# Performance work log

Hardware: AMD Instinct MI355X
Metric: run time of the kernel (lower is better)

## Reference

```python
import jax, jax.numpy as jnp
import numpy as np

B, S = 1, 2048
HIDDEN = 4096
NQ, NKV, HD = 32, 8, 128
EPS = 1e-06
THETA = 10000.0


def setup_inputs() -> dict:
    key = jax.random.key(0)
    k0, k1, k2 = jax.random.split(key, 3)
    hidden_states = jax.random.normal(k0, (B, S, HIDDEN), jnp.float32)
    Wqkv = jax.random.normal(k1, (HIDDEN, (NQ + 2 * NKV) * HD), jnp.float32) * 0.02
    Wo = jax.random.normal(k2, (NQ * HD, HIDDEN), jnp.float32) * 0.02
    q_gamma = jnp.ones((HD,), jnp.float32)
    k_gamma = jnp.ones((HD,), jnp.float32)
    positions = jnp.broadcast_to(jnp.arange(S, dtype=jnp.int32), (B, S))
    # neox-style rotary tables: half head_dim frequencies
    inv_freq = 1.0 / (THETA ** (jnp.arange(0, HD, 2, dtype=jnp.float32) / HD))  # [HD/2]
    ang = positions[..., None].astype(jnp.float32) * inv_freq                   # [B,S,HD/2]
    return {
        'positions': positions,
        'hidden_states': hidden_states,
        'Wqkv': Wqkv,
        'Wo': Wo,
        'q_gamma': q_gamma,
        'k_gamma': k_gamma,
        'cos': jnp.cos(ang),
        'sin': jnp.sin(ang),
    }


def _rmsnorm(x, gamma):
    # per-head RMSNorm over last dim (head_dim)
    return x * jax.lax.rsqrt(jnp.mean(x * x, axis=-1, keepdims=True) + EPS) * gamma


def _rope(x, cos, sin):
    # x: [B,S,h,HD], cos/sin: [B,S,HD/2]; rotate-half (neox) style
    x1, x2 = jnp.split(x, 2, axis=-1)
    c = cos[:, :, None, :]
    s = sin[:, :, None, :]
    return jnp.concatenate([x1 * c - x2 * s, x2 * c + x1 * s], axis=-1)


def reference(positions, hidden_states, Wqkv, Wo, q_gamma, k_gamma, cos, sin):
    b, s, _ = hidden_states.shape
    qkv = hidden_states @ Wqkv                                  # [B,S,(NQ+2NKV)*HD]
    q, k, v = jnp.split(qkv, [NQ * HD, (NQ + NKV) * HD], axis=-1)
    q = _rmsnorm(q.reshape(b, s, NQ, HD), q_gamma)
    k = _rmsnorm(k.reshape(b, s, NKV, HD), k_gamma)
    v = v.reshape(b, s, NKV, HD)
    q = _rope(q, cos, sin)
    k = _rope(k, cos, sin)
    R = NQ // NKV                                               # GQA group size
    qg = q.reshape(b, s, NKV, R, HD)
    scores = jnp.einsum('bsgrd,btgd->bgrst', qg, k) * (HD ** -0.5)
    causal = jnp.tril(jnp.ones((s, s), bool))
    scores = jnp.where(causal, scores, jnp.finfo(scores.dtype).min)
    probs = jax.nn.softmax(scores, axis=-1)
    attn = jnp.einsum('bgrst,btgd->bsgrd', probs, v).reshape(b, s, NQ * HD)
    return attn @ Wo
```

## Files before the change

### kernel.cpp

```cpp
#include <hip/hip_runtime.h>
#include <hip/hip_bf16.h>


#define S_LEN   2048
#define HIDDEN  4096
#define NQ      32
#define NKV     8
#define HD      128
#define QKV_DIM 6144
#define NQHD    4096
#define K_OFF   4096
#define V_OFF   5120
#define EPSF    1e-6f

typedef _Float16 half8 __attribute__((ext_vector_type(8)));
typedef _Float16 half4v __attribute__((ext_vector_type(4)));
typedef _Float16 half2v __attribute__((ext_vector_type(2)));
typedef float floatx4 __attribute__((ext_vector_type(4)));

__device__ __forceinline__ void gload_lds16(const void* g, void* l) {
    __builtin_amdgcn_global_load_lds(
        (const __attribute__((address_space(1))) unsigned int*)g,
        (__attribute__((address_space(3))) unsigned int*)l, 16, 0, 0);
}

__global__ __launch_bounds__(256) void conv_f32_f16(const float* __restrict__ src,
                                                    _Float16* __restrict__ dst) {
    const size_t i = ((size_t)blockIdx.x * 256 + threadIdx.x) * 8;
    float4 a = *(const float4*)(src + i);
    float4 b = *(const float4*)(src + i + 4);
    half8 h;
    h[0] = (_Float16)a.x; h[1] = (_Float16)a.y; h[2] = (_Float16)a.z; h[3] = (_Float16)a.w;
    h[4] = (_Float16)b.x; h[5] = (_Float16)b.y; h[6] = (_Float16)b.z; h[7] = (_Float16)b.w;
    *(half8*)(dst + i) = h;
}

__global__ __launch_bounds__(256) void conv_w_transpose(const float* __restrict__ src,
                                                        _Float16* __restrict__ dst,
                                                        int N, int K) {
    __shared__ float T[64][65];
    const int tid = threadIdx.x;
    const int n0 = blockIdx.x * 64, k0 = blockIdx.y * 64;
    const int rr = tid >> 4, cc = (tid & 15) * 4;
    #pragma unroll
    for (int l = 0; l < 4; ++l) {
        const int r = rr + l * 16;
        *(float4*)&T[r][cc] = *(const float4*)(src + (size_t)(k0 + r) * N + n0 + cc);
    }
    __syncthreads();
    #pragma unroll
    for (int l = 0; l < 4; ++l) {
        const int rn = rr + l * 16;
        half4v h;
        h[0] = (_Float16)T[cc + 0][rn];
        h[1] = (_Float16)T[cc + 1][rn];
        h[2] = (_Float16)T[cc + 2][rn];
        h[3] = (_Float16)T[cc + 3][rn];
        *(half4v*)(dst + (size_t)(n0 + rn) * K + k0 + cc) = h;
    }
}

#define MFMA_PH(MB, NB)                                                        \
    asm volatile("s_waitcnt lgkmcnt(0)" ::: "memory");                         \
    __builtin_amdgcn_sched_barrier(0);                                         \
    __builtin_amdgcn_s_setprio(1);                                             \
    _Pragma("unroll")                                                          \
    for (int ks = 0; ks < 2; ++ks)                                             \
        _Pragma("unroll")                                                      \
        for (int mt = 0; mt < 4; ++mt)                                         \
            _Pragma("unroll")                                                  \
            for (int nt = 0; nt < 2; ++nt)                                     \
                acc[(MB) + mt][(NB) + nt] =                                    \
                    __builtin_amdgcn_mfma_f32_16x16x32_f16(                    \
                        af[mt][ks], bf[(NB) + nt][ks],                         \
                        acc[(MB) + mt][(NB) + nt], 0, 0, 0);                   \
    __builtin_amdgcn_s_setprio(0);                                             \
    __builtin_amdgcn_sched_barrier(0);

#define READ_AF(H)                                                             \
    _Pragma("unroll")                                                          \
    for (int mt = 0; mt < 4; ++mt) {                                           \
        const char* p_ = aB + ((H) * 64 + mt * 16 + fl) * 128;                 \
        af[mt][0] = *(const half8*)(p_ + cs0);                                 \
        af[mt][1] = *(const half8*)(p_ + cs1);                                 \
    }

#define READ_BF(NB)                                                            \
    _Pragma("unroll")                                                          \
    for (int j = 0; j < 2; ++j) {                                              \
        const char* p_ = bB + (((NB) + j) * 16 + fl) * 128;                    \
        bf[(NB) + j][0] = *(const half8*)(p_ + cs0);                           \
        bf[(NB) + j][1] = *(const half8*)(p_ + cs1);                           \
    }

#define PHBAR asm volatile("s_barrier" ::: "memory")

template <typename CT, int BN>
__global__ __launch_bounds__(512, 2) void gemm_8ph(const _Float16* __restrict__ A,
                                                   const _Float16* __restrict__ Bt,
                                                   CT* __restrict__ C,
                                                   int K, int ldc) {
    constexpr int NI = BN / 64;
    constexpr int NBH = BN / 128;

    __shared__ _Float16 sA[2][2][128 * 64];
    __shared__ _Float16 sB[2][NBH][128 * 64];

    const int tid = threadIdx.x;
    const int wave = tid >> 6, lane = tid & 63;
    const int fl = lane & 15, quad = lane >> 4;
    const int wmh = wave >> 2;
    const int wn  = (wave & 3) * (BN / 4);

    const int m0 = blockIdx.y * 256, n0 = blockIdx.x * BN;

    const int srow = lane >> 3;
    const int sch  = ((lane & 7) ^ srow) * 8;

    auto stA = [&](int buf, int kt, int h) {
        const _Float16* s = A + (size_t)(m0 + h * 128 + wave * 8 + srow) * K
                            + kt * 64 + sch;
        _Float16* d = &sA[buf][h][(wave * 8) * 64];
        gload_lds16(s, d);
        gload_lds16(s + (size_t)64 * K, d + 64 * 64);
    };
    auto stB = [&](int buf, int kt, int h) {
        const _Float16* s = Bt + (size_t)(n0 + h * 128 + wave * 8 + srow) * K
                            + kt * 64 + sch;
        _Float16* d = &sB[buf][h][(wave * 8) * 64];
        gload_lds16(s, d);
        gload_lds16(s + (size_t)64 * K, d + 64 * 64);
    };

    floatx4 acc[8][NI] = {};
    const int cs0 = (quad ^ (fl & 7)) << 4;
    const int cs1 = ((4 + quad) ^ (fl & 7)) << 4;

    if constexpr (BN == 256) {
        stA(0, 0, 0); stA(0, 0, 1);
        stB(0, 0, 0); stB(0, 0, 1);
        stB(1, 1, 0); stB(1, 1, 1);
    } else {
        stA(0, 0, 0); stA(0, 0, 1);
        stB(0, 0, 0);
        stB(1, 1, 0);
    }

    const int NT = K >> 6;
    for (int t = 0; t < NT; ++t) {
        const int cur = t & 1;
        const char* aB = (const char*)&sA[cur][wmh][0];
        const char* bB = (BN == 256)
            ? (const char*)&sB[cur][wn >> 7][0] + (size_t)(wn & 64) * 128
            : (const char*)&sB[cur][0][0] + (size_t)wn * 128;

        half8 af[4][2], bf[NI][2];

        if constexpr (BN == 256)
            asm volatile("s_waitcnt vmcnt(4)\n\ts_barrier" ::: "memory");
        else
            asm volatile("s_waitcnt vmcnt(2)\n\ts_barrier" ::: "memory");

        if constexpr (BN == 256) {
            READ_AF(0)
            READ_BF(0)
            if (t + 1 < NT) stA(cur ^ 1, t + 1, 0);
            PHBAR;
            MFMA_PH(0, 0)
            PHBAR;
            READ_BF(2)
            if (t + 1 < NT) stA(cur ^ 1, t + 1, 1);
            PHBAR;
            MFMA_PH(0, 2)
            PHBAR;
            READ_AF(1)
            if (t + 2 < NT) stB(cur, t + 2, 0);
            PHBAR;
            MFMA_PH(4, 0)
            PHBAR;
            if (t + 2 < NT) stB(cur, t + 2, 1);
            PHBAR;
            MFMA_PH(4, 2)
        } else {
            READ_AF(0)
            READ_BF(0)
            if (t + 1 < NT) stA(cur ^ 1, t + 1, 0);
            PHBAR;
            MFMA_PH(0, 0)
            PHBAR;
            READ_AF(1)
            if (t + 1 < NT) stA(cur ^ 1, t + 1, 1);
            if (t + 2 < NT) stB(cur, t + 2, 0);
            PHBAR;
            MFMA_PH(4, 0)
        }
    }

    #pragma unroll
    for (int mi = 0; mi < 8; ++mi)
        #pragma unroll
        for (int ni = 0; ni < NI; ++ni)
            #pragma unroll
            for (int r = 0; r < 4; ++r)
                C[(size_t)(m0 + wmh * 128 + mi * 16 + quad * 4 + r) * ldc
                  + n0 + wn + ni * 16 + fl] = (CT)acc[mi][ni][r];
}

#undef MFMA_PH
#undef READ_AF
#undef READ_BF
#undef PHBAR

__global__ __launch_bounds__(256) void rmsnorm_rope_w(_Float16* __restrict__ qkv,
                                                      const float* __restrict__ qg,
                                                      const float* __restrict__ kg,
                                                      const float* __restrict__ cosb,
                                                      const float* __restrict__ sinb) {
    const int s = blockIdx.x;
    const int wave = threadIdx.x >> 6, lane = threadIdx.x & 63;
    const float c  = cosb[s * 64 + lane];
    const float sn = sinb[s * 64 + lane];

    #pragma unroll
    for (int hi = 0; hi < 10; ++hi) {
        const int h = hi * 4 + wave;
        const bool isq = (h < NQ);
        _Float16* base = qkv + (size_t)s * QKV_DIM
                         + (isq ? h * HD : K_OFF + (h - NQ) * HD);
        float x1 = (float)base[lane];
        float x2 = (float)base[lane + 64];
        float ss = x1 * x1 + x2 * x2;
        #pragma unroll
        for (int o = 32; o; o >>= 1) ss += __shfl_xor(ss, o);
        float rms = rsqrtf(ss * (1.0f / (float)HD) + EPSF);
        const float* g = isq ? qg : kg;
        float xn1 = x1 * rms * g[lane];
        float xn2 = x2 * rms * g[lane + 64];
        base[lane]      = (_Float16)(xn1 * c - xn2 * sn);
        base[lane + 64] = (_Float16)(xn2 * c + xn1 * sn);
    }
}

#define FAM 32
#define FAN 64
#define LQK 136
#define LVP 68

__global__ __launch_bounds__(256, 2) void flash_attn_gqa(
        const _Float16* __restrict__ qkv, _Float16* __restrict__ attn) {
    __shared__ __align__(16) _Float16 Ks[FAN][LQK];
    __shared__ __align__(16) _Float16 Vt[HD][LVP];
    __shared__ __align__(16) _Float16 Ps[4][FAM][LVP];

    const int tid = threadIdx.x;
    const int wave = tid >> 6, lane = tid & 63;
    const int fl = lane & 15, quad = lane >> 4;

    const int bd = blockIdx.x;
    const int c = bd & 255, sflip = bd >> 8;
    const int qt = sflip ? 63 - (c & 63) : (c & 63);
    const int kvh = (sflip << 2) + (c >> 6);
    const int h = kvh * 4 + wave;
    const int m0 = qt * FAM;
    const float scale = 0.08838834764831845f;

    half8 qf[2][4];
    #pragma unroll
    for (int mt = 0; mt < 2; ++mt)
        #pragma unroll
        for (int ks = 0; ks < 4; ++ks)
            qf[mt][ks] = *(const half8*)(qkv
                + (size_t)(m0 + mt * 16 + fl) * QKV_DIM + h * HD + ks * 32 + quad * 8);

    float m_prev[2][4], l_prev[2][4];
    #pragma unroll
    for (int mt = 0; mt < 2; ++mt)
        #pragma unroll
        for (int r = 0; r < 4; ++r) { m_prev[mt][r] = -1e30f; l_prev[mt][r] = 0.f; }
    floatx4 oacc[2][8] = {};

    const int tmax = (m0 + FAM - 1) / FAN;
    for (int t = 0; t <= tmax; ++t) {
        const int n0 = t * FAN;
        __syncthreads();

        #pragma unroll
        for (int l = 0; l < 4; ++l) {
            const int f = tid + l * 256;
            const int r = f >> 4, c8 = (f & 15) * 8;
            *(half8*)&Ks[r][c8] = *(const half8*)(qkv
                + (size_t)(n0 + r) * QKV_DIM + K_OFF + kvh * HD + c8);
        }
        {
            const int p = tid & 31, g0 = tid >> 5;
            #pragma unroll
            for (int gi = 0; gi < 2; ++gi) {
                const int g = g0 + gi * 8;
                const _Float16* v0p = qkv + (size_t)(n0 + 2 * p) * QKV_DIM
                                      + V_OFF + kvh * HD + 8 * g;
                half8 va = *(const half8*)v0p;
                half8 vb = *(const half8*)(v0p + QKV_DIM);
                #pragma unroll
                for (int i = 0; i < 8; ++i) {
                    half2v hh; hh[0] = va[i]; hh[1] = vb[i];
                    *(half2v*)&Vt[8 * g + i][2 * p] = hh;
                }
            }
        }
        __syncthreads();

        floatx4 sacc[2][4] = {};
        __builtin_amdgcn_s_setprio(1);
        #pragma unroll
        for (int ks = 0; ks < 4; ++ks)
            #pragma unroll
            for (int nt = 0; nt < 4; ++nt) {
                half8 bf = *(const half8*)&Ks[nt * 16 + fl][ks * 32 + quad * 8];
                sacc[0][nt] = __builtin_amdgcn_mfma_f32_16x16x32_f16(
                    qf[0][ks], bf, sacc[0][nt], 0, 0, 0);
                sacc[1][nt] = __builtin_amdgcn_mfma_f32_16x16x32_f16(
                    qf[1][ks], bf, sacc[1][nt], 0, 0, 0);
            }
        __builtin_amdgcn_s_setprio(0);

        const bool diag = (t == tmax);
        float mx[2][4];
        #pragma unroll
        for (int mt = 0; mt < 2; ++mt)
            #pragma unroll
            for (int r = 0; r < 4; ++r) mx[mt][r] = -1e30f;
        #pragma unroll
        for (int mt = 0; mt < 2; ++mt)
            #pragma unroll
            for (int nt = 0; nt < 4; ++nt)
                #pragma unroll
                for (int r = 0; r < 4; ++r) {
                    float sv = sacc[mt][nt][r] * scale;
                    if (diag && (n0 + nt * 16 + fl > m0 + mt * 16 + quad * 4 + r))
                        sv = -1e30f;
                    sacc[mt][nt][r] = sv;
                    mx[mt][r] = fmaxf(mx[mt][r], sv);
                }
        #pragma unroll
        for (int mt = 0; mt < 2; ++mt)
            #pragma unroll
            for (int r = 0; r < 4; ++r)
                #pragma unroll
                for (int o = 8; o; o >>= 1)
                    mx[mt][r] = fmaxf(mx[mt][r], __shfl_xor(mx[mt][r], o));

        float alpha[2][4], rs[2][4];
        #pragma unroll
        for (int mt = 0; mt < 2; ++mt)
            #pragma unroll
            for (int r = 0; r < 4; ++r) {
                float nm = fmaxf(m_prev[mt][r], mx[mt][r]);
                alpha[mt][r] = __expf(m_prev[mt][r] - nm);
                m_prev[mt][r] = nm;
                rs[mt][r] = 0.f;
            }
        #pragma unroll
        for (int mt = 0; mt < 2; ++mt)
            #pragma unroll
            for (int nt = 0; nt < 4; ++nt)
                #pragma unroll
                for (int r = 0; r < 4; ++r) {
                    float p = __expf(sacc[mt][nt][r] - m_prev[mt][r]);
                    rs[mt][r] += p;
                    Ps[wave][mt * 16 + quad * 4 + r][nt * 16 + fl] = (_Float16)p;
                }
        #pragma unroll
        for (int mt = 0; mt < 2; ++mt)
            #pragma unroll
            for (int r = 0; r < 4; ++r) {
                #pragma unroll
                for (int o = 8; o; o >>= 1) rs[mt][r] += __shfl_xor(rs[mt][r], o);
                l_prev[mt][r] = l_prev[mt][r] * alpha[mt][r] + rs[mt][r];
            }
        #pragma unroll
        for (int mt = 0; mt < 2; ++mt)
            #pragma unroll
            for (int dt = 0; dt < 8; ++dt)
                #pragma unroll
                for (int r = 0; r < 4; ++r) oacc[mt][dt][r] *= alpha[mt][r];

        __builtin_amdgcn_s_setprio(1);
        #pragma unroll
        for (int ks2 = 0; ks2 < 2; ++ks2) {
            half8 pa[2];
            #pragma unroll
            for (int mt = 0; mt < 2; ++mt) {
                half4v plo = *(const half4v*)&Ps[wave][mt * 16 + fl][ks2 * 32 + quad * 8];
                half4v phi = *(const half4v*)&Ps[wave][mt * 16 + fl][ks2 * 32 + quad * 8 + 4];
                pa[mt] = __builtin_shufflevector(plo, phi, 0, 1, 2, 3, 4, 5, 6, 7);
            }
            #pragma unroll
            for (int dt = 0; dt < 8; ++dt) {
                half4v vlo = *(const half4v*)&Vt[dt * 16 + fl][ks2 * 32 + quad * 8];
                half4v vhi = *(const half4v*)&Vt[dt * 16 + fl][ks2 * 32 + quad * 8 + 4];
                half8 vb = __builtin_shufflevector(vlo, vhi, 0, 1, 2, 3, 4, 5, 6, 7);
                oacc[0][dt] = __builtin_amdgcn_mfma_f32_16x16x32_f16(
                    pa[0], vb, oacc[0][dt], 0, 0, 0);
                oacc[1][dt] = __builtin_amdgcn_mfma_f32_16x16x32_f16(
                    pa[1], vb, oacc[1][dt], 0, 0, 0);
            }
        }
        __builtin_amdgcn_s_setprio(0);
    }

    #pragma unroll
    for (int mt = 0; mt < 2; ++mt) {
        float linv[4];
        #pragma unroll
        for (int r = 0; r < 4; ++r) linv[r] = 1.0f / l_prev[mt][r];
        #pragma unroll
        for (int dt = 0; dt < 8; ++dt)
            #pragma unroll
            for (int r = 0; r < 4; ++r)
                attn[(size_t)(m0 + mt * 16 + quad * 4 + r) * NQHD
                     + h * HD + dt * 16 + fl] = (_Float16)(oacc[mt][dt][r] * linv[r]);
    }
}

extern "C" void kernel_launch(void* const* d_in, const int* in_sizes, int n_in,
                              void* d_out, int out_size, void* d_ws, size_t ws_size,
                              hipStream_t stream) {
    const float* hidden = (const float*)d_in[1];
    const float* Wqkv   = (const float*)d_in[2];
    const float* Wo     = (const float*)d_in[3];
    const float* qg     = (const float*)d_in[4];
    const float* kg     = (const float*)d_in[5];
    const float* cosb   = (const float*)d_in[6];
    const float* sinb   = (const float*)d_in[7];
    float* out = (float*)d_out;

    _Float16* buf0  = (_Float16*)d_ws;
    _Float16* wT    = buf0 + (size_t)S_LEN * HIDDEN;
    _Float16* qkv16 = (_Float16*)d_out;
    _Float16* attn16 = buf0;

    conv_f32_f16<<<(S_LEN * HIDDEN) / 2048, 256, 0, stream>>>(hidden, buf0);
    conv_w_transpose<<<dim3(QKV_DIM / 64, HIDDEN / 64), 256, 0, stream>>>(
        Wqkv, wT, QKV_DIM, HIDDEN);
    gemm_8ph<_Float16, 256><<<dim3(QKV_DIM / 256, S_LEN / 256), 512, 0, stream>>>(
        buf0, wT, qkv16, HIDDEN, QKV_DIM);
    rmsnorm_rope_w<<<S_LEN, 256, 0, stream>>>(qkv16, qg, kg, cosb, sinb);
    flash_attn_gqa<<<dim3((S_LEN / FAM) * NKV), 256, 0, stream>>>(qkv16, attn16);
    conv_w_transpose<<<dim3(HIDDEN / 64, NQHD / 64), 256, 0, stream>>>(
        Wo, wT, HIDDEN, NQHD);
    gemm_8ph<float, 128><<<dim3(HIDDEN / 128, S_LEN / 256), 512, 0, stream>>>(
        attn16, wT, out, NQHD, HIDDEN);
}
```

Baseline: 547.5 us.

## Split flash attention across 8 waves with register-prefetched K/V and lazy rescale

The attention kernel now runs 512 threads per block, with each wave handling one head and one 16-row query tile instead of two tiles. The next K/V tile is loaded into registers while the current tile is computed, which overlaps global loads with MFMA work. Softmax now uses exp2 with a log2e-folded scale, and the running max and accumulator are rescaled only when the max grows past a threshold. This removes per-iteration rescale work but relies on fp32 headroom for the deferred rescale, and the added registers may reduce occupancy.

```diff
diff --git a/kernel.cpp b/kernel.cpp
--- a/kernel.cpp
+++ b/kernel.cpp
@@ -245,181 +245,174 @@
 #define FAN 64
 #define LQK 136
 #define LVP 68
-
-__global__ __launch_bounds__(256, 2) void flash_attn_gqa(
+#define THR_L2 8.0f
+
+__global__ __launch_bounds__(512, 4) void flash_attn_gqa8(
         const _Float16* __restrict__ qkv, _Float16* __restrict__ attn) {
     __shared__ __align__(16) _Float16 Ks[FAN][LQK];
     __shared__ __align__(16) _Float16 Vt[HD][LVP];
-    __shared__ __align__(16) _Float16 Ps[4][FAM][LVP];
+    __shared__ __align__(16) _Float16 Ps[8][16][LVP];
 
     const int tid = threadIdx.x;
     const int wave = tid >> 6, lane = tid & 63;
     const int fl = lane & 15, quad = lane >> 4;
+    const int hw = wave >> 1, mt = wave & 1;
 
     const int bd = blockIdx.x;
     const int c = bd & 255, sflip = bd >> 8;
     const int qt = sflip ? 63 - (c & 63) : (c & 63);
     const int kvh = (sflip << 2) + (c >> 6);
-    const int h = kvh * 4 + wave;
+    const int h = kvh * 4 + hw;
     const int m0 = qt * FAM;
-    const float scale = 0.08838834764831845f;
-
-    half8 qf[2][4];
-    #pragma unroll
-    for (int mt = 0; mt < 2; ++mt)
-        #pragma unroll
-        for (int ks = 0; ks < 4; ++ks)
-            qf[mt][ks] = *(const half8*)(qkv
-                + (size_t)(m0 + mt * 16 + fl) * QKV_DIM + h * HD + ks * 32 + quad * 8);
-
-    float m_prev[2][4], l_prev[2][4];
-    #pragma unroll
-    for (int mt = 0; mt < 2; ++mt)
-        #pragma unroll
-        for (int r = 0; r < 4; ++r) { m_prev[mt][r] = -1e30f; l_prev[mt][r] = 0.f; }
-    floatx4 oacc[2][8] = {};
+    const float scl2 = 0.12751879523209784f;
+
+    half8 qf[4];
+    #pragma unroll
+    for (int ks = 0; ks < 4; ++ks)
+        qf[ks] = *(const half8*)(qkv
+            + (size_t)(m0 + mt * 16 + fl) * QKV_DIM + h * HD + ks * 32 + quad * 8);
+
+    const int vp = tid & 31, vg = tid >> 5;
+
+    float m_prev[4], l_prev[4];
+    #pragma unroll
+    for (int r = 0; r < 4; ++r) { m_prev[r] = -1e30f; l_prev[r] = 0.f; }
+    floatx4 oacc[8] = {};
 
     const int tmax = (m0 + FAM - 1) / FAN;
+
+    half8 kreg[2], vra, vrb;
+    {
+        #pragma unroll
+        for (int l = 0; l < 2; ++l) {
+            const int f = tid + l * 512;
+            kreg[l] = *(const half8*)(qkv + (size_t)(f >> 4) * QKV_DIM
+                       + K_OFF + kvh * HD + (f & 15) * 8);
+        }
+        const _Float16* v0p = qkv + (size_t)(2 * vp) * QKV_DIM
+                              + V_OFF + kvh * HD + 8 * vg;
+        vra = *(const half8*)v0p;
+        vrb = *(const half8*)(v0p + QKV_DIM);
+    }
+
     for (int t = 0; t <= tmax; ++t) {
         const int n0 = t * FAN;
         __syncthreads();
 
         #pragma unroll
-        for (int l = 0; l < 4; ++l) {
-            const int f = tid + l * 256;
-            const int r = f >> 4, c8 = (f & 15) * 8;
-            *(half8*)&Ks[r][c8] = *(const half8*)(qkv
-                + (size_t)(n0 + r) * QKV_DIM + K_OFF + kvh * HD + c8);
-        }
-        {
-            const int p = tid & 31, g0 = tid >> 5;
-            #pragma unroll
-            for (int gi = 0; gi < 2; ++gi) {
-                const int g = g0 + gi * 8;
-                const _Float16* v0p = qkv + (size_t)(n0 + 2 * p) * QKV_DIM
-                                      + V_OFF + kvh * HD + 8 * g;
-                half8 va = *(const half8*)v0p;
-                half8 vb = *(const half8*)(v0p + QKV_DIM);
-                #pragma unroll
-                for (int i = 0; i < 8; ++i) {
-                    half2v hh; hh[0] = va[i]; hh[1] = vb[i];
-                    *(half2v*)&Vt[8 * g + i][2 * p] = hh;
-                }
-            }
+        for (int l = 0; l < 2; ++l) {
+            const int f = tid + l * 512;
+            *(half8*)&Ks[f >> 4][(f & 15) * 8] = kreg[l];
+        }
+        #pragma unroll
+        for (int i = 0; i < 8; ++i) {
+            half2v hh; hh[0] = vra[i]; hh[1] = vrb[i];
+            *(half2v*)&Vt[8 * vg + i][2 * vp] = hh;
         }
         __syncthreads();
 
-        floatx4 sacc[2][4] = {};
+        if (t < tmax) {
+            const int n1 = n0 + FAN;
+            #pragma unroll
+            for (int l = 0; l < 2; ++l) {
+                const int f = tid + l * 512;
+                kreg[l] = *(const half8*)(qkv + (size_t)(n1 + (f >> 4)) * QKV_DIM
+                           + K_OFF + kvh * HD + (f & 15) * 8);
+            }
+            const _Float16* v1p = qkv + (size_t)(n1 + 2 * vp) * QKV_DIM
+                                  + V_OFF + kvh * HD + 8 * vg;
+            vra = *(const half8*)v1p;
+            vrb = *(const half8*)(v1p + QKV_DIM);
+        }
+
+        floatx4 sacc[4] = {};
         __builtin_amdgcn_s_setprio(1);
         #pragma unroll
         for (int ks = 0; ks < 4; ++ks)
             #pragma unroll
             for (int nt = 0; nt < 4; ++nt) {
                 half8 bf = *(const half8*)&Ks[nt * 16 + fl][ks * 32 + quad * 8];
-                sacc[0][nt] = __builtin_amdgcn_mfma_f32_16x16x32_f16(
-                    qf[0][ks], bf, sacc[0][nt], 0, 0, 0);
-                sacc[1][nt] = __builtin_amdgcn_mfma_f32_16x16x32_f16(
-                    qf[1][ks], bf, sacc[1][nt], 0, 0, 0);
+                sacc[nt] = __builtin_amdgcn_mfma_f32_16x16x32_f16(
+                    qf[ks], bf, sacc[nt], 0, 0, 0);
             }
         __builtin_amdgcn_s_setprio(0);
 
         const bool diag = (t == tmax);
-        float mx[2][4];
-        #pragma unroll
-        for (int mt = 0; mt < 2; ++mt)
-            #pragma unroll
-            for (int r = 0; r < 4; ++r) mx[mt][r] = -1e30f;
-        #pragma unroll
-        for (int mt = 0; mt < 2; ++mt)
-            #pragma unroll
-            for (int nt = 0; nt < 4; ++nt)
+        float mx[4] = {-1e30f, -1e30f, -1e30f, -1e30f};
+        #pragma unroll
+        for (int nt = 0; nt < 4; ++nt)
+            #pragma unroll
+            for (int r = 0; r < 4; ++r) {
+                float sv = sacc[nt][r] * scl2;
+                if (diag && (n0 + nt * 16 + fl > m0 + mt * 16 + quad * 4 + r))
+                    sv = -1e30f;
+                sacc[nt][r] = sv;
+                mx[r] = fmaxf(mx[r], sv);
+            }
+        #pragma unroll
+        for (int r = 0; r < 4; ++r)
+            #pragma unroll
+            for (int o = 8; o; o >>= 1)
+                mx[r] = fmaxf(mx[r], __shfl_xor(mx[r], o));
+
+        bool grow = false;
+        #pragma unroll
+        for (int r = 0; r < 4; ++r) grow |= (mx[r] > m_prev[r] + THR_L2);
+        if (__any(grow ? 1 : 0)) {
+            #pragma unroll
+            for (int r = 0; r < 4; ++r) {
+                float nm = fmaxf(m_prev[r], mx[r]);
+                float a = exp2f(m_prev[r] - nm);
+                m_prev[r] = nm;
+                l_prev[r] *= a;
                 #pragma unroll
-                for (int r = 0; r < 4; ++r) {
-                    float sv = sacc[mt][nt][r] * scale;
-                    if (diag && (n0 + nt * 16 + fl > m0 + mt * 16 + quad * 4 + r))
-                        sv = -1e30f;
-                    sacc[mt][nt][r] = sv;
-                    mx[mt][r] = fmaxf(mx[mt][r], sv);
-                }
-        #pragma unroll
-        for (int mt = 0; mt < 2; ++mt)
-            #pragma unroll
-            for (int r = 0; r < 4; ++r)
-                #pragma unroll
-                for (int o = 8; o; o >>= 1)
-                    mx[mt][r] = fmaxf(mx[mt][r], __shfl_xor(mx[mt][r], o));
-
-        float alpha[2][4], rs[2][4];
-        #pragma unroll
-        for (int mt = 0; mt < 2; ++mt)
+                for (int dt = 0; dt < 8; ++dt) oacc[dt][r] *= a;
+            }
+        }
+
+        float rs[4] = {0.f, 0.f, 0.f, 0.f};
+        #pragma unroll
+        for (int nt = 0; nt < 4; ++nt)
             #pragma unroll
             for (int r = 0; r < 4; ++r) {
-                float nm = fmaxf(m_prev[mt][r], mx[mt][r]);
-                alpha[mt][r] = __expf(m_prev[mt][r] - nm);
-                m_prev[mt][r] = nm;
-                rs[mt][r] = 0.f;
-            }
-        #pragma unroll
-        for (int mt = 0; mt < 2; ++mt)
-            #pragma unroll
-            for (int nt = 0; nt < 4; ++nt)
-                #pragma unroll
-                for (int r = 0; r < 4; ++r) {
-                    float p = __expf(sacc[mt][nt][r] - m_prev[mt][r]);
-                    rs[mt][r] += p;
-                    Ps[wave][mt * 16 + quad * 4 + r][nt * 16 + fl] = (_Float16)p;
-                }
-        #pragma unroll
-        for (int mt = 0; mt < 2; ++mt)
-            #pragma unroll
-            for (int r = 0; r < 4; ++r) {
-                #pragma unroll
-                for (int o = 8; o; o >>= 1) rs[mt][r] += __shfl_xor(rs[mt][r], o);
-                l_prev[mt][r] = l_prev[mt][r] * alpha[mt][r] + rs[mt][r];
-            }
-        #pragma unroll
-        for (int mt = 0; mt < 2; ++mt)
-            #pragma unroll
-            for (int dt = 0; dt < 8; ++dt)
-                #pragma unroll
-                for (int r = 0; r < 4; ++r) oacc[mt][dt][r] *= alpha[mt][r];
+                float p = exp2f(sacc[nt][r] - m_prev[r]);
+                rs[r] += p;
+                Ps[wave][quad * 4 + r][nt * 16 + fl] = (_Float16)p;
+            }
+        #pragma unroll
+        for (int r = 0; r < 4; ++r) {
+            #pragma unroll
+            for (int o = 8; o; o >>= 1) rs[r] += __shfl_xor(rs[r], o);
+            l_prev[r] += rs[r];
+        }
 
         __builtin_amdgcn_s_setprio(1);
         #pragma unroll
         for (int ks2 = 0; ks2 < 2; ++ks2) {
-            half8 pa[2];
-            #pragma unroll
-            for (int mt = 0; mt < 2; ++mt) {
-                half4v plo = *(const half4v*)&Ps[wave][mt * 16 + fl][ks2 * 32 + quad * 8];
-                half4v phi = *(const half4v*)&Ps[wave][mt * 16 + fl][ks2 * 32 + quad * 8 + 4];
-                pa[mt] = __builtin_shufflevector(plo, phi, 0, 1, 2, 3, 4, 5, 6, 7);
-            }
+            half4v plo = *(const half4v*)&Ps[wave][fl][ks2 * 32 + quad * 8];
+            half4v phi = *(const half4v*)&Ps[wave][fl][ks2 * 32 + quad * 8 + 4];
+            half8 pa = __builtin_shufflevector(plo, phi, 0, 1, 2, 3, 4, 5, 6, 7);
             #pragma unroll
             for (int dt = 0; dt < 8; ++dt) {
                 half4v vlo = *(const half4v*)&Vt[dt * 16 + fl][ks2 * 32 + quad * 8];
                 half4v vhi = *(const half4v*)&Vt[dt * 16 + fl][ks2 * 32 + quad * 8 + 4];
                 half8 vb = __builtin_shufflevector(vlo, vhi, 0, 1, 2, 3, 4, 5, 6, 7);
-                oacc[0][dt] = __builtin_amdgcn_mfma_f32_16x16x32_f16(
-                    pa[0], vb, oacc[0][dt], 0, 0, 0);
-                oacc[1][dt] = __builtin_amdgcn_mfma_f32_16x16x32_f16(
-                    pa[1], vb, oacc[1][dt], 0, 0, 0);
+                oacc[dt] = __builtin_amdgcn_mfma_f32_16x16x32_f16(
+                    pa, vb, oacc[dt], 0, 0, 0);
             }
         }
         __builtin_amdgcn_s_setprio(0);
     }
 
-    #pragma unroll
-    for (int mt = 0; mt < 2; ++mt) {
-        float linv[4];
-        #pragma unroll
-        for (int r = 0; r < 4; ++r) linv[r] = 1.0f / l_prev[mt][r];
-        #pragma unroll
-        for (int dt = 0; dt < 8; ++dt)
-            #pragma unroll
-            for (int r = 0; r < 4; ++r)
-                attn[(size_t)(m0 + mt * 16 + quad * 4 + r) * NQHD
-                     + h * HD + dt * 16 + fl] = (_Float16)(oacc[mt][dt][r] * linv[r]);
-    }
+    float linv[4];
+    #pragma unroll
+    for (int r = 0; r < 4; ++r) linv[r] = 1.0f / l_prev[r];
+    #pragma unroll
+    for (int dt = 0; dt < 8; ++dt)
+        #pragma unroll
+        for (int r = 0; r < 4; ++r)
+            attn[(size_t)(m0 + mt * 16 + quad * 4 + r) * NQHD
+                 + h * HD + dt * 16 + fl] = (_Float16)(oacc[dt][r] * linv[r]);
 }
 
 extern "C" void kernel_launch(void* const* d_in, const int* in_sizes, int n_in,
@@ -445,7 +438,7 @@
     gemm_8ph<_Float16, 256><<<dim3(QKV_DIM / 256, S_LEN / 256), 512, 0, stream>>>(
         buf0, wT, qkv16, HIDDEN, QKV_DIM);
     rmsnorm_rope_w<<<S_LEN, 256, 0, stream>>>(qkv16, qg, kg, cosb, sinb);
-    flash_attn_gqa<<<dim3((S_LEN / FAM) * NKV), 256, 0, stream>>>(qkv16, attn16);
+    flash_attn_gqa8<<<dim3((S_LEN / FAM) * NKV), 512, 0, stream>>>(qkv16, attn16);
     conv_w_transpose<<<dim3(HIDDEN / 64, NQHD / 64), 256, 0, stream>>>(
         Wo, wT, HIDDEN, NQHD);
     gemm_8ph<float, 128><<<dim3(HIDDEN / 128, S_LEN / 256), 512, 0, stream>>>(
```

Result: no change. 540.6 us (-1.3%).
